# Kernel optimization log

Hardware: AMD Instinct MI355X
Metric: run time of the kernel (lower is better)

The kernel has to match this reference:

```python
import jax, jax.numpy as jnp
import numpy as np

B, S, D, VOCAB, K = 32, 128, 300, 20000, 8


def setup_inputs() -> dict:
    key = jax.random.key(0)
    ks = jax.random.split(key, 12)
    return {
        "words": jax.random.normal(ks[0], (B, S, D), jnp.float32),
        "lengths": jax.random.randint(ks[1], (B,), S // 2, S + 1),
        "vocab": jax.random.normal(ks[2], (VOCAB, D), jnp.float32) * 0.1,
        "default_embed": jax.random.uniform(ks[3], (D,), jnp.float32),
        "W": jnp.eye(D, dtype=jnp.float32) + 0.01 * jax.random.normal(ks[4], (D, D), jnp.float32),
        "lstm_Wih": jax.random.normal(ks[5], (4 * D, D), jnp.float32) * 0.05,
        "lstm_Whh": jax.random.normal(ks[6], (4 * D, D), jnp.float32) * 0.05,
        "lstm_bih": jnp.zeros((4 * D,), jnp.float32),
        "lstm_bhh": jnp.zeros((4 * D,), jnp.float32),
        "rnn_Wih": jax.random.normal(ks[7], (D, D), jnp.float32) * 0.05,
        "rnn_Whh": jax.random.normal(ks[8], (D, D), jnp.float32) * 0.05,
        "rnn_bih": jnp.zeros((D,), jnp.float32),
        "rnn_bhh": jnp.zeros((D,), jnp.float32),
    }


def _forward(words, lengths, vocab, default_embed, W,
             lstm_Wih, lstm_Whh, lstm_bih, lstm_bhh,
             rnn_Wih, rnn_Whh, rnn_bih, rnn_bhh):
    b, s, d = words.shape
    # --- NormalizeWordsModel (tagger) ---
    C = jnp.concatenate([vocab.T, default_embed[:, None]], axis=1)  # [D, V+1]
    P = jax.nn.softmax(jnp.einsum("bsd,de,ev->bsv", words, W, C), axis=-1)  # [B,S,V+1]
    V = P[..., -1:] * words + jnp.einsum("bsv,vd->bsd", P[..., :-1], vocab)  # [B,S,D]

    # --- LSTM encoder, final hidden at true length (packed-sequence semantics) ---
    valid = (jnp.arange(s)[None, :] < lengths[:, None])  # [B,S]

    def lstm_step(carry, xs):
        h, c = carry
        x_t, v_t = xs  # [B,D], [B]
        gates = x_t @ lstm_Wih.T + lstm_bih + h @ lstm_Whh.T + lstm_bhh  # [B,4D]
        i, f, g, o = jnp.split(gates, 4, axis=-1)
        c_new = jax.nn.sigmoid(f) * c + jax.nn.sigmoid(i) * jnp.tanh(g)
        h_new = jax.nn.sigmoid(o) * jnp.tanh(c_new)
        m = v_t[:, None]
        h = jnp.where(m, h_new, h)
        c = jnp.where(m, c_new, c)
        return (h, c), None

    h0 = jnp.zeros((b, d), V.dtype)
    (q, _), _ = jax.lax.scan(lstm_step, (h0, h0),
                             (jnp.swapaxes(V, 0, 1), valid.T))  # q: [B,D]

    # --- InstructionsDecoder: RNNCell applied K times to the same input q ---
    def rnn_step(h, _):
        h2 = jnp.tanh(q @ rnn_Wih.T + rnn_bih + h @ rnn_Whh.T + rnn_bhh)
        return h2, h2

    _, H = jax.lax.scan(rnn_step, h0, None, length=K)  # [K,B,D]
    H = jnp.swapaxes(H, 0, 1)  # [B,K,D]

    # --- masked softmax attention readout ---
    scores = jnp.einsum("bkd,bsd->bks", H, V)  # [B,K,S]
    scores = jnp.where(valid[:, None, :], scores, -jnp.inf)
    R = jnp.einsum("bks,bsd->bkd", jax.nn.softmax(scores, axis=-1), V)
    return R


def reference(words, lengths, vocab, default_embed, W,
              lstm_Wih, lstm_Whh, lstm_bih, lstm_bhh,
              rnn_Wih, rnn_Whh, rnn_bih, rnn_bhh):
    return _forward(words, lengths, vocab, default_embed, W,
                    lstm_Wih, lstm_Whh, lstm_bih, lstm_bhh,
                    rnn_Wih, rnn_Whh, rnn_bih, rnn_bhh)
```

## Files before the change

### kernel.cpp

```cpp
#include <hip/hip_runtime.h>


typedef unsigned short u16;
typedef unsigned int   u32;
typedef float  f32x4 __attribute__((ext_vector_type(4)));
typedef u32    u32x4 __attribute__((ext_vector_type(4)));
typedef __bf16 bf16x8 __attribute__((ext_vector_type(8)));
typedef _Float16 f16x2 __attribute__((ext_vector_type(2)));
typedef _Float16 f16x8 __attribute__((ext_vector_type(8)));

#define SCOPE_AGENT __HIP_MEMORY_SCOPE_AGENT

__device__ __forceinline__ float bf2f(u16 u) { return __uint_as_float(((u32)u) << 16); }
__device__ __forceinline__ u16 f2bf(float f) {
  u32 x = __float_as_uint(f);
  u32 r = (x + 0x7fffu + ((x >> 16) & 1u)) >> 16;
  return (u16)r;
}
__device__ __forceinline__ float sigm(float x) { return 1.f / (1.f + __expf(-x)); }
__device__ __forceinline__ u16 f2h(float f) {
  union { _Float16 h; u16 u; } cv; cv.h = (_Float16)f; return cv.u;
}
__device__ __forceinline__ float h2f(u16 u) {
  union { _Float16 h; u16 u; } cv; cv.u = u; return (float)cv.h;
}

template <int CTRL>
__device__ __forceinline__ float dppmv(float v) {
  return __uint_as_float(
      (u32)__builtin_amdgcn_mov_dpp((int)__float_as_uint(v), CTRL, 0xF, 0xF, true));
}

__device__ __forceinline__ void stage_chunk(const u16* __restrict__ pA,
                                            const u16* __restrict__ pB,
                                            int ci, u16* dst, int tid) {
  const u32x4* gA = (const u32x4*)pA + (size_t)ci * 1280;
  const u32x4* gB = (const u32x4*)pB + (size_t)ci * 1216;
  u32x4* sb = (u32x4*)dst;
#pragma unroll
  for (int i = 0; i < 5; i++) {
    int idx = tid + i * 512;
    if (idx < 2496) {
      const u32x4* g = (idx < 1280) ? (gA + idx) : (gB + (idx - 1280));
      __builtin_amdgcn_global_load_lds(
          (const __attribute__((address_space(1))) u32*)(const u32*)g,
          (__attribute__((address_space(3))) u32*)(u32*)(sb + idx), 16, 0, 0);
    }
  }
}

__device__ __forceinline__ void conv_seg(const void* src, u16* dst, int n, int is32,
                                         int t0, int stride) {
  if (is32) {
    const float* s = (const float*)src;
    for (int i = t0; i < n; i += stride) dst[i] = f2bf(s[i]);
  } else {
    const u16* s = (const u16*)src;
    for (int i = t0; i < n; i += stride) dst[i] = s[i];
  }
}

__global__ __launch_bounds__(256) void k_ingest(
    const void* words, const void* vocab, const void* de, const void* W,
    const void* lWih, const void* lWhh, const void* lbih, const void* lbhh,
    const void* rWih, const void* rWhh, const void* rbih, const void* rbhh,
    u16* cw, u16* cv, u16* cde, u16* cW, u16* cWih, u16* cWhh, u16* cbih, u16* cbhh,
    u16* crWih, u16* crWhh, u16* crbih, u16* crbhh, u32* flag, u32* seqz, u32* hbz) {
  __shared__ int s_is32;
  int tid = threadIdx.x;
  int vote = 0;
  if (tid < 64) {
    u32 w = ((const u32*)words)[tid];
    int e = (w >> 7) & 0xFF;
    vote = (e >= 100 && e <= 150) ? 1 : 0;
  }
  unsigned long long m = __ballot(vote);
  if (tid == 0) s_is32 = (__popcll(m) < 32) ? 1 : 0;
  __syncthreads();
  int is32 = s_is32;
  if (blockIdx.x == 0 && tid == 0) *flag = (u32)is32;
  int t0 = blockIdx.x * 256 + tid;
  int stride = gridDim.x * 256;
  if (t0 < 256) seqz[t0] = 0;
  if (t0 < 10240) hbz[t0] = 0;
  conv_seg(words, cw, 1228800, is32, t0, stride);
  conv_seg(vocab, cv, 6000000, is32, t0, stride);
  conv_seg(de, cde, 300, is32, t0, stride);
  conv_seg(W, cW, 90000, is32, t0, stride);
  conv_seg(lWih, cWih, 360000, is32, t0, stride);
  conv_seg(lWhh, cWhh, 360000, is32, t0, stride);
  conv_seg(lbih, cbih, 1200, is32, t0, stride);
  conv_seg(lbhh, cbhh, 1200, is32, t0, stride);
  conv_seg(rWih, crWih, 90000, is32, t0, stride);
  conv_seg(rWhh, crWhh, 90000, is32, t0, stride);
  conv_seg(rbih, crbih, 300, is32, t0, stride);
  conv_seg(rbhh, crbhh, 300, is32, t0, stride);
}

__global__ __launch_bounds__(256) void k_transpose_bf(const u16* __restrict__ in,
                                                      u16* __restrict__ out,
                                                      int J, int K) {
  __shared__ u16 t[32][33];
  int j0 = blockIdx.x * 32, k0 = blockIdx.y * 32;
  int lx = threadIdx.x & 31, ly = threadIdx.x >> 5;
  for (int r = ly; r < 32; r += 8) {
    int j = j0 + r, k = k0 + lx;
    t[r][lx] = (j < J && k < K) ? in[(size_t)j * K + k] : (u16)0;
  }
  __syncthreads();
  for (int r = ly; r < 32; r += 8) {
    int k = k0 + r, j = j0 + lx;
    if (k < K && j < J) out[(size_t)k * J + j] = t[lx][r];
  }
}

__global__ __launch_bounds__(256) void k_pack_w4(const u16* __restrict__ Whh,
                                                 u16* __restrict__ pW) {
  int idx = blockIdx.x * 256 + threadIdx.x;
  if (idx >= 16 * 25600) return;
  int bid = idx / 25600, r = idx % 25600;
  int t2 = r >> 9, lane = (r >> 3) & 63, j = r & 7;
  int nt = t2 / 10, kt = t2 % 10;
  int n = nt * 16 + (lane & 15);
  int gate = n / 20, dl = n % 20;
  int d0 = (bid < 15) ? 19 * bid : 285;
  int nd = (bid < 15) ? 19 : 15;
  int k = kt * 32 + ((lane >> 4) * 8) + j;
  u16 out = 0;
  if (dl < nd && k < 300) out = f2h(bf2f(Whh[(size_t)(gate * 300 + d0 + dl) * 300 + k]));
  pW[idx] = out;
}

__global__ __launch_bounds__(256) void k_pack_vocab(const u16* __restrict__ vocab,
                                                    u16* __restrict__ pA,
                                                    u16* __restrict__ pB) {
  __shared__ u16 sv[32][320];
  int ci = blockIdx.x, tid = threadIdx.x;
  for (int idx = tid; idx < 32 * 20; idx += 256) {
    int v = idx / 20, k = 300 + (idx - v * 20);
    sv[v][k] = 0;
  }
  for (int idx = tid; idx < 32 * 300; idx += 256) {
    int v = idx / 300, k = idx - v * 300;
    sv[v][k] = vocab[(size_t)(ci * 32 + v) * 300 + k];
  }
  __syncthreads();
  for (int idx = tid; idx < 10240; idx += 256) {
    int j = idx & 7, lane = (idx >> 3) & 63, t2 = idx >> 9;
    int kk = t2 % 10, h = t2 / 10;
    int v = h * 16 + (lane & 15);
    int k = kk * 32 + ((lane >> 4)) * 8 + j;
    pA[(size_t)ci * 10240 + (size_t)idx] = sv[v][k];
  }
  for (int idx = tid; idx < 9728; idx += 256) {
    int j = idx & 7, lane = (idx >> 3) & 63, nc = idx >> 9;
    int v = (lane >> 4) * 8 + j;
    int n = nc * 16 + (lane & 15);
    pB[(size_t)ci * 9728 + (size_t)idx] = sv[v][n];
  }
}

__global__ __launch_bounds__(256) void k_xw(const u16* __restrict__ words,
                                            const u16* __restrict__ W,
                                            u16* __restrict__ X) {
  __shared__ float As[300][33];
  int n0 = blockIdx.x * 128;
  int r0 = blockIdx.y * 32;
  int tid = threadIdx.x;
  for (int idx = tid; idx < 32 * 300; idx += 256) {
    int r = idx / 300, k = idx - r * 300;
    As[k][r] = bf2f(words[(size_t)(r0 + r) * 300 + k]);
  }
  __syncthreads();
  int j = n0 + (tid & 127);
  int rh = (tid >> 7) * 16;
  float acc[16];
#pragma unroll
  for (int i = 0; i < 16; i++) acc[i] = 0.f;
  if (j < 300) {
    for (int k = 0; k < 300; k++) {
      float bw = bf2f(W[(size_t)k * 300 + j]);
#pragma unroll
      for (int i = 0; i < 16; i++) acc[i] += As[k][rh + i] * bw;
    }
  }
  if (j < 320) {
#pragma unroll
    for (int i = 0; i < 16; i++) {
      float v = (j < 300) ? acc[i] : 0.f;
      X[(size_t)(r0 + rh + i) * 320 + j] = f2bf(v);
    }
  }
}

__global__ __launch_bounds__(512, 2) void k_softmax_v(
    const u16* __restrict__ X, const u16* __restrict__ pA, const u16* __restrict__ pB,
    u16* __restrict__ pAcc, float* __restrict__ pML) {
  __shared__ __align__(16) u16 chunk[2][19968];
  __shared__ __align__(16) float ptbuf[8 * 576];
  int bid = blockIdx.x;
  int sl = bid & 7, b = bid >> 3;
  int tid = threadIdx.x;
  int w = tid >> 6, lane = tid & 63;
  int quad = lane >> 4, n16 = lane & 15;
  int cs = (sl == 0) ? 0 : 79 + (sl - 1) * 78;
  int nch = (sl == 0) ? 79 : 78;

  int rowA = b * 128 + w * 16 + n16;
  const bf16x8* Xrow = (const bf16x8*)(X + (size_t)rowA * 320);
  bf16x8 afr[10];
#pragma unroll
  for (int kk = 0; kk < 10; kk++) afr[kk] = Xrow[kk * 4 + quad];

  f32x4 acc[19];
#pragma unroll
  for (int i = 0; i < 19; i++) { acc[i][0] = 0.f; acc[i][1] = 0.f; acc[i][2] = 0.f; acc[i][3] = 0.f; }
  f32x4 mrun, lrun;
#pragma unroll
  for (int c = 0; c < 4; c++) { mrun[c] = -1e30f; lrun[c] = 0.f; }
  float* myPt = ptbuf + w * 576;

  stage_chunk(pA, pB, cs, &chunk[0][0], tid);
  __syncthreads();

  int cur = 0;
  for (int ic = 0; ic < nch; ic++) {
    if (ic + 1 < nch) stage_chunk(pA, pB, cs + ic + 1, &chunk[cur ^ 1][0], tid);
    const bf16x8* bufA = (const bf16x8*)&chunk[cur][0];
    const bf16x8* bufB = (const bf16x8*)&chunk[cur][10240];
    f32x4 L0, L1;
#pragma unroll
    for (int c = 0; c < 4; c++) { L0[c] = 0.f; L1[c] = 0.f; }
#pragma unroll
    for (int kk = 0; kk < 10; kk++) {
      L0 = __builtin_amdgcn_mfma_f32_16x16x32_bf16(afr[kk], bufA[kk * 64 + lane], L0, 0, 0, 0);
      L1 = __builtin_amdgcn_mfma_f32_16x16x32_bf16(afr[kk], bufA[(10 + kk) * 64 + lane], L1, 0, 0, 0);
    }
    f32x4 t;
#pragma unroll
    for (int c = 0; c < 4; c++) {
      float x = fmaxf(L0[c], L1[c]);
      x = fmaxf(x, dppmv<0xB1>(x));
      x = fmaxf(x, dppmv<0x4E>(x));
      x = fmaxf(x, dppmv<0x141>(x));
      x = fmaxf(x, dppmv<0x140>(x));
      t[c] = x;
    }
    f32x4 mnew, al, P0v, P1v, rs;
#pragma unroll
    for (int c = 0; c < 4; c++) {
      mnew[c] = fmaxf(mrun[c], t[c]);
      al[c] = __expf(mrun[c] - mnew[c]);
      P0v[c] = __expf(L0[c] - mnew[c]);
      P1v[c] = __expf(L1[c] - mnew[c]);
      rs[c] = P0v[c] + P1v[c];
    }
#pragma unroll
    for (int c = 0; c < 4; c++) {
      float x = rs[c];
      x += dppmv<0xB1>(x);
      x += dppmv<0x4E>(x);
      x += dppmv<0x141>(x);
      x += dppmv<0x140>(x);
      rs[c] = x;
    }
#pragma unroll
    for (int c = 0; c < 4; c++) { lrun[c] = lrun[c] * al[c] + rs[c]; mrun[c] = mnew[c]; }
#pragma unroll
    for (int r = 0; r < 4; r++) {
      myPt[(quad * 4 + r) * 36 + n16] = P0v[r];
      myPt[(quad * 4 + r) * 36 + 16 + n16] = P1v[r];
    }
    f32x4 plo = *(const f32x4*)(myPt + n16 * 36 + quad * 8);
    f32x4 phi = *(const f32x4*)(myPt + n16 * 36 + quad * 8 + 4);
    bf16x8 paf;
#pragma unroll
    for (int c = 0; c < 4; c++) { paf[c] = (__bf16)plo[c]; paf[c + 4] = (__bf16)phi[c]; }
#pragma unroll
    for (int nc = 0; nc < 19; nc++) {
      f32x4 a = acc[nc];
#pragma unroll
      for (int c = 0; c < 4; c++) a[c] *= al[c];
      acc[nc] = __builtin_amdgcn_mfma_f32_16x16x32_bf16(paf, bufB[nc * 64 + lane], a, 0, 0, 0);
    }
    __syncthreads();
    cur ^= 1;
  }

  size_t prow = (size_t)sl * 4096 + (size_t)b * 128 + w * 16;
  if (n16 == 0) {
#pragma unroll
    for (int r = 0; r < 4; r++) {
      pML[(prow + quad * 4 + r) * 2 + 0] = mrun[r];
      pML[(prow + quad * 4 + r) * 2 + 1] = lrun[r];
    }
  }
#pragma unroll
  for (int nc = 0; nc < 19; nc++)
#pragma unroll
    for (int r = 0; r < 4; r++)
      pAcc[(prow + quad * 4 + r) * 304 + nc * 16 + n16] = f2bf(acc[nc][r]);
}

__global__ __launch_bounds__(320) void k_combine(
    const u16* __restrict__ pAcc, const float* __restrict__ pML,
    const u16* __restrict__ X, const u16* __restrict__ de,
    const u16* __restrict__ words, u16* __restrict__ Vout) {
  __shared__ float red[320];
  __shared__ float fs[8];
  __shared__ float sinv, sw;
  int row = blockIdx.x, tid = threadIdx.x;
  float p = 0.f;
  if (tid < 300) p = bf2f(X[(size_t)row * 320 + tid]) * bf2f(de[tid]);
  red[tid] = p;
  __syncthreads();
  if (tid == 0) {
    float d = 0.f;
    for (int i = 0; i < 300; i++) d += red[i];
    float mv[8], lv[8], ms = -1e30f;
    for (int s = 0; s < 8; s++) {
      mv[s] = pML[((size_t)s * 4096 + row) * 2];
      lv[s] = pML[((size_t)s * 4096 + row) * 2 + 1];
      ms = fmaxf(ms, mv[s]);
    }
    float mf = fmaxf(ms, d);
    float pd = __expf(d - mf);
    float l = pd;
    for (int s = 0; s < 8; s++) {
      float f = __expf(mv[s] - mf);
      fs[s] = f;
      l += lv[s] * f;
    }
    sinv = 1.f / l;
    sw = pd / l;
  }
  __syncthreads();
  float v = 0.f;
  if (tid < 300) {
    float a = 0.f;
#pragma unroll
    for (int s = 0; s < 8; s++)
      a += bf2f(pAcc[((size_t)s * 4096 + row) * 304 + tid]) * fs[s];
    v = a * sinv + sw * bf2f(words[(size_t)row * 300 + tid]);
  }
  Vout[(size_t)row * 320 + tid] = f2bf(v);
}

__global__ __launch_bounds__(256) void k_xg(const u16* __restrict__ Vb,
                                            const u16* __restrict__ WihT,
                                            const u16* __restrict__ bih,
                                            const u16* __restrict__ bhh,
                                            float* __restrict__ xg) {
  __shared__ float As[300][33];
  int n0 = blockIdx.x * 128;
  int r0 = blockIdx.y * 32;
  int tid = threadIdx.x;
  for (int idx = tid; idx < 32 * 300; idx += 256) {
    int r = idx / 300, k = idx - r * 300;
    As[k][r] = bf2f(Vb[(size_t)(r0 + r) * 320 + k]);
  }
  __syncthreads();
  int j = n0 + (tid & 127);
  if (j >= 1200) return;
  int rh = (tid >> 7) * 16;
  float acc[16];
#pragma unroll
  for (int i = 0; i < 16; i++) acc[i] = 0.f;
  for (int k = 0; k < 300; k++) {
    float bw = bf2f(WihT[(size_t)k * 1200 + j]);
#pragma unroll
    for (int i = 0; i < 16; i++) acc[i] += As[k][rh + i] * bw;
  }
  float bias = bf2f(bih[j]) + bf2f(bhh[j]);
#pragma unroll
  for (int i = 0; i < 16; i++)
    xg[(size_t)(r0 + rh + i) * 1200 + j] = acc[i] + bias;
}

__global__ __launch_bounds__(320, 1) void k_lstm2(
    const float* __restrict__ xg, const u16* __restrict__ pW,
    const int* __restrict__ lengths, u16* __restrict__ hb, u32* __restrict__ seq) {
  __shared__ float gl[32][84];
  __shared__ int s_maxlen;
  int bid = blockIdx.x, tid = threadIdx.x;
  int w = tid >> 6, lane = tid & 63;
  int quad = lane >> 4, n16 = lane & 15;
  int d0 = (bid < 15) ? 19 * bid : 285;
  int nd = (bid < 15) ? 19 : 15;
  {
    int lv = (tid < 32) ? lengths[tid] : 0;
    for (int off2 = 1; off2 < 32; off2 <<= 1) {
      int o = __shfl_xor(lv, off2, 64);
      lv = lv > o ? lv : o;
    }
    if (tid == 0) s_maxlen = lv;
  }
  f16x8 bf[10];
  const u32x4* pw4 = (const u32x4*)(pW + (size_t)bid * 25600);
#pragma unroll
  for (int kt = 0; kt < 10; kt++)
    bf[kt] = __builtin_bit_cast(f16x8, pw4[(w * 10 + kt) * 64 + lane]);
  int b0 = tid / 20, dl0 = tid - b0 * 20;
  int b1 = (tid + 320) / 20, dl1 = (tid + 320) - b1 * 20;
  bool a0 = dl0 < nd, a1 = dl1 < nd;
  int len0 = lengths[b0], len1 = lengths[b1];
  int dim0 = d0 + dl0, dim1 = d0 + dl1;
  int sa0 = (((b0 >> 4) * 10 + (dim0 >> 5)) * 64 + ((dim0 >> 3) & 3) * 16 + (b0 & 15)) * 8 + (dim0 & 7);
  int sa1 = (((b1 >> 4) * 10 + (dim1 >> 5)) * 64 + ((dim1 >> 3) & 3) * 16 + (b1 & 15)) * 8 + (dim1 & 7);
  float c0 = 0.f, h0 = 0.f, c1 = 0.f, h1 = 0.f;
  __syncthreads();
  int maxlen = s_maxlen;
  for (int t = 0; t < maxlen; t++) {
    if (tid < 16) {
      while (__hip_atomic_load(&seq[tid * 16], __ATOMIC_ACQUIRE, SCOPE_AGENT) < (u32)t)
        __builtin_amdgcn_s_sleep(2);
    }
    __syncthreads();
    float xv00 = 0.f, xv01 = 0.f, xv02 = 0.f, xv03 = 0.f;
    float xv10 = 0.f, xv11 = 0.f, xv12 = 0.f, xv13 = 0.f;
    const float* xr0 = xg + ((size_t)b0 * 128 + t) * 1200 + dim0;
    const float* xr1 = xg + ((size_t)b1 * 128 + t) * 1200 + dim1;
    if (a0) { xv00 = xr0[0]; xv01 = xr0[300]; xv02 = xr0[600]; xv03 = xr0[900]; }
    if (a1) { xv10 = xr1[0]; xv11 = xr1[300]; xv12 = xr1[600]; xv13 = xr1[900]; }
    const u32x4* hbt = (const u32x4*)hb + (size_t)(t & 1) * 1280;
    u32x4 af[2][10];
#pragma unroll
    for (int mt = 0; mt < 2; mt++)
#pragma unroll
      for (int kt = 0; kt < 10; kt++)
        af[mt][kt] = hbt[(mt * 10 + kt) * 64 + lane];
#pragma unroll
    for (int mt = 0; mt < 2; mt++) {
      f32x4 C;
      C[0] = 0.f; C[1] = 0.f; C[2] = 0.f; C[3] = 0.f;
#pragma unroll
      for (int kt = 0; kt < 10; kt++)
        C = __builtin_amdgcn_mfma_f32_16x16x32_f16(
            __builtin_bit_cast(f16x8, af[mt][kt]), bf[kt], C, 0, 0, 0);
#pragma unroll
      for (int rr = 0; rr < 4; rr++)
        gl[mt * 16 + quad * 4 + rr][w * 16 + n16] = C[rr];
    }
    __syncthreads();
    u16* hbw = hb + (size_t)((t + 1) & 1) * 10240;
    if (a0) {
      float gi = gl[b0][dl0] + xv00, gf = gl[b0][20 + dl0] + xv01;
      float gg = gl[b0][40 + dl0] + xv02, go = gl[b0][60 + dl0] + xv03;
      if (t < len0) {
        c0 = sigm(gf) * c0 + sigm(gi) * tanhf(gg);
        h0 = sigm(go) * tanhf(c0);
      }
      hbw[sa0] = f2h(h0);
    }
    if (a1) {
      float gi = gl[b1][dl1] + xv10, gf = gl[b1][20 + dl1] + xv11;
      float gg = gl[b1][40 + dl1] + xv12, go = gl[b1][60 + dl1] + xv13;
      if (t < len1) {
        c1 = sigm(gf) * c1 + sigm(gi) * tanhf(gg);
        h1 = sigm(go) * tanhf(c1);
      }
      hbw[sa1] = f2h(h1);
    }
    __syncthreads();
    if (tid == 0)
      __hip_atomic_store(&seq[bid * 16], (u32)(t + 1), __ATOMIC_RELEASE, SCOPE_AGENT);
  }
}

__global__ __launch_bounds__(320) void k_rnn(
    const u16* __restrict__ hb, const int* __restrict__ lengths,
    const u16* __restrict__ rWihT, const u16* __restrict__ rWhhT,
    const u16* __restrict__ rbih, const u16* __restrict__ rbhh,
    float* __restrict__ H) {
  __shared__ float qs[304], h2[304], base[304];
  __shared__ int s_maxlen;
  int b = blockIdx.x, tid = threadIdx.x;
  {
    int lv = (tid < 32) ? lengths[tid] : 0;
    for (int off2 = 1; off2 < 32; off2 <<= 1) {
      int o = __shfl_xor(lv, off2, 64);
      lv = lv > o ? lv : o;
    }
    if (tid == 0) s_maxlen = lv;
  }
  __syncthreads();
  int buf = s_maxlen & 1;
  if (tid < 304) {
    float q = 0.f;
    if (tid < 300) {
      int dim = tid;
      int idx = (((b >> 4) * 10 + (dim >> 5)) * 64 + ((dim >> 3) & 3) * 16 + (b & 15)) * 8 + (dim & 7);
      q = h2f(hb[(size_t)buf * 10240 + idx]);
    }
    qs[tid] = q;
    h2[tid] = 0.f;
  }
  __syncthreads();
  if (tid < 300) {
    float a = bf2f(rbih[tid]) + bf2f(rbhh[tid]);
    for (int k = 0; k < 300; k++) a += qs[k] * bf2f(rWihT[(size_t)k * 300 + tid]);
    base[tid] = a;
  }
  __syncthreads();
  for (int s = 0; s < 8; s++) {
    float nv = 0.f;
    if (tid < 300) {
      float a = base[tid];
      for (int k = 0; k < 300; k++) a += h2[k] * bf2f(rWhhT[(size_t)k * 300 + tid]);
      nv = tanhf(a);
    }
    __syncthreads();
    if (tid < 300) {
      h2[tid] = nv;
      H[((size_t)b * 8 + s) * 300 + tid] = nv;
    }
    __syncthreads();
  }
}

__global__ __launch_bounds__(256) void k_attn(const float* __restrict__ H,
                                              const u16* __restrict__ Vb,
                                              const int* __restrict__ lengths,
                                              const u32* __restrict__ flag,
                                              void* __restrict__ dout) {
  __shared__ float Hs[8][304];
  __shared__ float sc[8][128];
  __shared__ float wsum[8];
  int b = blockIdx.x, tid = threadIdx.x;
  int len = lengths[b];
  int is32 = (int)*flag;
  for (int idx = tid; idx < 8 * 300; idx += 256) {
    int k = idx / 300, j = idx - k * 300;
    Hs[k][j] = H[((size_t)b * 8 + k) * 300 + j];
  }
  __syncthreads();
  for (int s = tid; s < len; s += 256) {
    const u16* vr = Vb + (size_t)(b * 128 + s) * 320;
    float a[8];
#pragma unroll
    for (int k = 0; k < 8; k++) a[k] = 0.f;
    for (int j = 0; j < 300; j++) {
      float v = bf2f(vr[j]);
#pragma unroll
      for (int k = 0; k < 8; k++) a[k] += Hs[k][j] * v;
    }
#pragma unroll
    for (int k = 0; k < 8; k++) sc[k][s] = a[k];
  }
  __syncthreads();
  if (tid < 8) {
    float m = -1e30f;
    for (int s = 0; s < len; s++) m = fmaxf(m, sc[tid][s]);
    float l = 0.f;
    for (int s = 0; s < len; s++) { float e = __expf(sc[tid][s] - m); sc[tid][s] = e; l += e; }
    wsum[tid] = 1.f / l;
  }
  __syncthreads();
  int k = tid >> 5, jl = tid & 31;
  for (int j = jl; j < 300; j += 32) {
    float a = 0.f;
    for (int s = 0; s < len; s++) a += sc[k][s] * bf2f(Vb[(size_t)(b * 128 + s) * 320 + j]);
    float val = a * wsum[k];
    size_t o = ((size_t)b * 8 + k) * 300 + j;
    if (is32) ((float*)dout)[o] = val;
    else ((u16*)dout)[o] = f2bf(val);
  }
}

extern "C" void kernel_launch(void* const* d_in, const int* in_sizes, int n_in,
                              void* d_out, int out_size, void* d_ws, size_t ws_size,
                              hipStream_t stream) {
  (void)in_sizes; (void)n_in; (void)out_size; (void)ws_size;
  const void* words = d_in[0];
  const int* lengths = (const int*)d_in[1];
  const void* vocab = d_in[2];
  const void* de = d_in[3];
  const void* W = d_in[4];
  const void* lWih = d_in[5];
  const void* lWhh = d_in[6];
  const void* lbih = d_in[7];
  const void* lbhh = d_in[8];
  const void* rWih = d_in[9];
  const void* rWhh = d_in[10];
  const void* rbih = d_in[11];
  const void* rbhh = d_in[12];

  char* basep = (char*)d_ws;
  size_t off = 0;
  auto take = [&](size_t bytes) -> char* {
    char* p = basep + off;
    off += (bytes + 255) & ~(size_t)255;
    return p;
  };
  u16* cw    = (u16*)take(1228800 * 2);
  u16* cv    = (u16*)take(6000000 * 2);
  u16* cde   = (u16*)take(300 * 2);
  u16* cW    = (u16*)take(90000 * 2);
  u16* cWih  = (u16*)take(360000 * 2);
  u16* cWhh  = (u16*)take(360000 * 2);
  u16* cbih  = (u16*)take(1200 * 2);
  u16* cbhh  = (u16*)take(1200 * 2);
  u16* crWih = (u16*)take(90000 * 2);
  u16* crWhh = (u16*)take(90000 * 2);
  u16* crbih = (u16*)take(300 * 2);
  u16* crbhh = (u16*)take(300 * 2);
  u32* flag  = (u32*)take(256);
  u16*   X     = (u16*)take((size_t)4096 * 320 * 2);
  u16*   Vb    = (u16*)take((size_t)4096 * 320 * 2);
  u16*   WihT  = (u16*)take((size_t)300 * 1200 * 2);
  u16*   pW4   = (u16*)take((size_t)16 * 25600 * 2);
  u16*   rWihT = (u16*)take((size_t)300 * 300 * 2);
  u16*   rWhhT = (u16*)take((size_t)300 * 300 * 2);
  u16*   pAcc  = (u16*)take((size_t)8 * 4096 * 304 * 2);
  float* pML   = (float*)take((size_t)8 * 4096 * 2 * 4);
  float* H     = (float*)take((size_t)32 * 8 * 300 * 4);
  u16*   hb    = (u16*)take((size_t)2 * 10240 * 2);
  u32*   seq   = (u32*)take((size_t)4096 * 4);
  char* ureg = take((size_t)25000192);
  u16*   pA = (u16*)ureg;
  u16*   pB = (u16*)(ureg + (size_t)625 * 10240 * 2);
  float* xg = (float*)ureg;

  k_ingest<<<4096, 256, 0, stream>>>(words, vocab, de, W, lWih, lWhh, lbih, lbhh,
                                     rWih, rWhh, rbih, rbhh,
                                     cw, cv, cde, cW, cWih, cWhh, cbih, cbhh,
                                     crWih, crWhh, crbih, crbhh, flag, seq, (u32*)hb);
  k_transpose_bf<<<dim3(38, 10), 256, 0, stream>>>(cWih, WihT, 1200, 300);
  k_transpose_bf<<<dim3(10, 10), 256, 0, stream>>>(crWih, rWihT, 300, 300);
  k_transpose_bf<<<dim3(10, 10), 256, 0, stream>>>(crWhh, rWhhT, 300, 300);
  k_pack_w4<<<1600, 256, 0, stream>>>(cWhh, pW4);
  k_pack_vocab<<<625, 256, 0, stream>>>(cv, pA, pB);
  k_xw<<<dim3(3, 128), 256, 0, stream>>>(cw, cW, X);
  k_softmax_v<<<256, 512, 0, stream>>>(X, pA, pB, pAcc, pML);
  k_combine<<<4096, 320, 0, stream>>>(pAcc, pML, X, cde, cw, Vb);
  k_xg<<<dim3(10, 128), 256, 0, stream>>>(Vb, WihT, cbih, cbhh, xg);
  k_lstm2<<<16, 320, 0, stream>>>(xg, pW4, lengths, hb, seq);
  k_rnn<<<32, 320, 0, stream>>>(hb, lengths, rWihT, rWhhT, crbih, crbhh, H);
  k_attn<<<32, 256, 0, stream>>>(H, Vb, lengths, flag, d_out);
}
```

Baseline: 1.065 ms.

## Split LSTM recurrence into two independent batch groups of eight blocks

The recurrent LSTM kernel is restructured so the 32 sequences form two independent groups of 16. Each group gets 8 blocks of 640 threads, each block owning 38 hidden dims. Blocks now synchronize only with the 8 blocks of their own group, and each group stops at its own max length. The hidden-state exchange buffer is split per group, and the Whh packing and the RNN kernel's reads are adjusted to match. This cuts the per-step cross-block barrier fan-in and lets the shorter group finish early, in exchange for more threads per block and MFMA tiles padded out to 40 columns per gate.

New measurement: 990.6 us. 1.08x faster.

```diff
diff --git a/kernel.cpp b/kernel.cpp
--- a/kernel.cpp
+++ b/kernel.cpp
@@ -114,20 +114,25 @@
   }
 }
 
-__global__ __launch_bounds__(256) void k_pack_w4(const u16* __restrict__ Whh,
+__global__ __launch_bounds__(256) void k_pack_w8(const u16* __restrict__ Whh,
                                                  u16* __restrict__ pW) {
   int idx = blockIdx.x * 256 + threadIdx.x;
-  if (idx >= 16 * 25600) return;
-  int bid = idx / 25600, r = idx % 25600;
-  int t2 = r >> 9, lane = (r >> 3) & 63, j = r & 7;
-  int nt = t2 / 10, kt = t2 % 10;
-  int n = nt * 16 + (lane & 15);
-  int gate = n / 20, dl = n % 20;
-  int d0 = (bid < 15) ? 19 * bid : 285;
-  int nd = (bid < 15) ? 19 : 15;
-  int k = kt * 32 + ((lane >> 4) * 8) + j;
+  if (idx >= 409600) return;
+  int bid = idx / 51200;
+  int r = idx - bid * 51200;
+  int j = r & 7;
+  int lane = (r >> 3) & 63;
+  int t2 = r >> 9;
+  int kt = t2 % 10, w = t2 / 10;
+  int n16 = lane & 15, quad = lane >> 4;
+  int n = w * 16 + n16;
+  int gate = n / 40, dl = n - gate * 40;
+  int nd = (bid < 7) ? 38 : 34;
+  int dim = 38 * bid + dl;
+  int k = kt * 32 + quad * 8 + j;
   u16 out = 0;
-  if (dl < nd && k < 300) out = f2h(bf2f(Whh[(size_t)(gate * 300 + d0 + dl) * 300 + k]));
+  if (dl < nd && k < 300)
+    out = f2h(bf2f(Whh[(size_t)(gate * 300 + dim) * 300 + k]));
   pW[idx] = out;
 }
 
@@ -377,93 +382,77 @@
     xg[(size_t)(r0 + rh + i) * 1200 + j] = acc[i] + bias;
 }
 
-__global__ __launch_bounds__(320, 1) void k_lstm2(
+__global__ __launch_bounds__(640, 1) void k_lstm7(
     const float* __restrict__ xg, const u16* __restrict__ pW,
     const int* __restrict__ lengths, u16* __restrict__ hb, u32* __restrict__ seq) {
-  __shared__ float gl[32][84];
+  __shared__ float gl[16][164];
   __shared__ int s_maxlen;
-  int bid = blockIdx.x, tid = threadIdx.x;
+  int bidx = blockIdx.x;
+  int mg = bidx >> 3, bid = bidx & 7;
+  int tid = threadIdx.x;
   int w = tid >> 6, lane = tid & 63;
   int quad = lane >> 4, n16 = lane & 15;
-  int d0 = (bid < 15) ? 19 * bid : 285;
-  int nd = (bid < 15) ? 19 : 15;
+  int nd = (bid < 7) ? 38 : 34;
   {
-    int lv = (tid < 32) ? lengths[tid] : 0;
-    for (int off2 = 1; off2 < 32; off2 <<= 1) {
+    int lv = (tid < 16) ? lengths[mg * 16 + tid] : 0;
+    for (int off2 = 1; off2 < 16; off2 <<= 1) {
       int o = __shfl_xor(lv, off2, 64);
       lv = lv > o ? lv : o;
     }
     if (tid == 0) s_maxlen = lv;
   }
   f16x8 bf[10];
-  const u32x4* pw4 = (const u32x4*)(pW + (size_t)bid * 25600);
+  const u32x4* pw4 = (const u32x4*)(pW + (size_t)bid * 51200);
 #pragma unroll
   for (int kt = 0; kt < 10; kt++)
     bf[kt] = __builtin_bit_cast(f16x8, pw4[(w * 10 + kt) * 64 + lane]);
-  int b0 = tid / 20, dl0 = tid - b0 * 20;
-  int b1 = (tid + 320) / 20, dl1 = (tid + 320) - b1 * 20;
-  bool a0 = dl0 < nd, a1 = dl1 < nd;
-  int len0 = lengths[b0], len1 = lengths[b1];
-  int dim0 = d0 + dl0, dim1 = d0 + dl1;
-  int sa0 = (((b0 >> 4) * 10 + (dim0 >> 5)) * 64 + ((dim0 >> 3) & 3) * 16 + (b0 & 15)) * 8 + (dim0 & 7);
-  int sa1 = (((b1 >> 4) * 10 + (dim1 >> 5)) * 64 + ((dim1 >> 3) & 3) * 16 + (b1 & 15)) * 8 + (dim1 & 7);
-  float c0 = 0.f, h0 = 0.f, c1 = 0.f, h1 = 0.f;
+  int b0 = tid / 40, dl = tid - b0 * 40;
+  bool a0 = dl < nd;
+  int bg = mg * 16 + b0;
+  int len0 = lengths[bg];
+  int dim = 38 * bid + dl;
+  int sa = (((dim >> 5)) * 64 + ((dim >> 3) & 3) * 16 + b0) * 8 + (dim & 7);
+  float c0 = 0.f, h0 = 0.f;
+  u32* myf = seq + (size_t)bidx * 16;
   __syncthreads();
   int maxlen = s_maxlen;
   for (int t = 0; t < maxlen; t++) {
-    if (tid < 16) {
-      while (__hip_atomic_load(&seq[tid * 16], __ATOMIC_ACQUIRE, SCOPE_AGENT) < (u32)t)
+    if (tid < 8) {
+      while (__hip_atomic_load(&seq[(mg * 8 + tid) * 16], __ATOMIC_ACQUIRE, SCOPE_AGENT) < (u32)t)
         __builtin_amdgcn_s_sleep(2);
     }
     __syncthreads();
-    float xv00 = 0.f, xv01 = 0.f, xv02 = 0.f, xv03 = 0.f;
-    float xv10 = 0.f, xv11 = 0.f, xv12 = 0.f, xv13 = 0.f;
-    const float* xr0 = xg + ((size_t)b0 * 128 + t) * 1200 + dim0;
-    const float* xr1 = xg + ((size_t)b1 * 128 + t) * 1200 + dim1;
-    if (a0) { xv00 = xr0[0]; xv01 = xr0[300]; xv02 = xr0[600]; xv03 = xr0[900]; }
-    if (a1) { xv10 = xr1[0]; xv11 = xr1[300]; xv12 = xr1[600]; xv13 = xr1[900]; }
-    const u32x4* hbt = (const u32x4*)hb + (size_t)(t & 1) * 1280;
-    u32x4 af[2][10];
-#pragma unroll
-    for (int mt = 0; mt < 2; mt++)
-#pragma unroll
-      for (int kt = 0; kt < 10; kt++)
-        af[mt][kt] = hbt[(mt * 10 + kt) * 64 + lane];
-#pragma unroll
-    for (int mt = 0; mt < 2; mt++) {
-      f32x4 C;
-      C[0] = 0.f; C[1] = 0.f; C[2] = 0.f; C[3] = 0.f;
-#pragma unroll
-      for (int kt = 0; kt < 10; kt++)
-        C = __builtin_amdgcn_mfma_f32_16x16x32_f16(
-            __builtin_bit_cast(f16x8, af[mt][kt]), bf[kt], C, 0, 0, 0);
-#pragma unroll
-      for (int rr = 0; rr < 4; rr++)
-        gl[mt * 16 + quad * 4 + rr][w * 16 + n16] = C[rr];
-    }
+    float xv0 = 0.f, xv1 = 0.f, xv2 = 0.f, xv3 = 0.f;
+    const float* xr0 = xg + ((size_t)bg * 128 + t) * 1200 + dim;
+    if (a0) { xv0 = xr0[0]; xv1 = xr0[300]; xv2 = xr0[600]; xv3 = xr0[900]; }
+    const u32x4* hbt = (const u32x4*)hb + (size_t)(mg * 2 + (t & 1)) * 640;
+    u32x4 af[10];
+#pragma unroll
+    for (int kt = 0; kt < 10; kt++)
+      af[kt] = hbt[kt * 64 + lane];
+    f32x4 C;
+    C[0] = 0.f; C[1] = 0.f; C[2] = 0.f; C[3] = 0.f;
+#pragma unroll
+    for (int kt = 0; kt < 10; kt++)
+      C = __builtin_amdgcn_mfma_f32_16x16x32_f16(
+          __builtin_bit_cast(f16x8, af[kt]), bf[kt], C, 0, 0, 0);
+#pragma unroll
+    for (int rr = 0; rr < 4; rr++)
+      gl[quad * 4 + rr][w * 16 + n16] = C[rr];
     __syncthreads();
-    u16* hbw = hb + (size_t)((t + 1) & 1) * 10240;
+    u16* hbw = hb + (size_t)(mg * 2 + ((t + 1) & 1)) * 5120;
     if (a0) {
-      float gi = gl[b0][dl0] + xv00, gf = gl[b0][20 + dl0] + xv01;
-      float gg = gl[b0][40 + dl0] + xv02, go = gl[b0][60 + dl0] + xv03;
+      float gi = gl[b0][dl] + xv0, gf = gl[b0][40 + dl] + xv1;
+      float gg = gl[b0][80 + dl] + xv2, go = gl[b0][120 + dl] + xv3;
       if (t < len0) {
         c0 = sigm(gf) * c0 + sigm(gi) * tanhf(gg);
         h0 = sigm(go) * tanhf(c0);
       }
-      hbw[sa0] = f2h(h0);
-    }
-    if (a1) {
-      float gi = gl[b1][dl1] + xv10, gf = gl[b1][20 + dl1] + xv11;
-      float gg = gl[b1][40 + dl1] + xv12, go = gl[b1][60 + dl1] + xv13;
-      if (t < len1) {
-        c1 = sigm(gf) * c1 + sigm(gi) * tanhf(gg);
-        h1 = sigm(go) * tanhf(c1);
-      }
-      hbw[sa1] = f2h(h1);
+      hbw[sa] = f2h(h0);
     }
     __syncthreads();
     if (tid == 0)
-      __hip_atomic_store(&seq[bid * 16], (u32)(t + 1), __ATOMIC_RELEASE, SCOPE_AGENT);
+      __hip_atomic_store(myf, (u32)(t + 1), __ATOMIC_RELEASE, SCOPE_AGENT);
   }
 }
 
@@ -475,9 +464,10 @@
   __shared__ float qs[304], h2[304], base[304];
   __shared__ int s_maxlen;
   int b = blockIdx.x, tid = threadIdx.x;
+  int mg = b >> 4;
   {
-    int lv = (tid < 32) ? lengths[tid] : 0;
-    for (int off2 = 1; off2 < 32; off2 <<= 1) {
+    int lv = (tid < 16) ? lengths[mg * 16 + tid] : 0;
+    for (int off2 = 1; off2 < 16; off2 <<= 1) {
       int o = __shfl_xor(lv, off2, 64);
       lv = lv > o ? lv : o;
     }
@@ -489,8 +479,8 @@
     float q = 0.f;
     if (tid < 300) {
       int dim = tid;
-      int idx = (((b >> 4) * 10 + (dim >> 5)) * 64 + ((dim >> 3) & 3) * 16 + (b & 15)) * 8 + (dim & 7);
-      q = h2f(hb[(size_t)buf * 10240 + idx]);
+      int idx = ((dim >> 5) * 64 + ((dim >> 3) & 3) * 16 + (b & 15)) * 8 + (dim & 7);
+      q = h2f(hb[(size_t)(mg * 2 + buf) * 5120 + idx]);
     }
     qs[tid] = q;
     h2[tid] = 0.f;
@@ -608,13 +598,13 @@
   u16*   X     = (u16*)take((size_t)4096 * 320 * 2);
   u16*   Vb    = (u16*)take((size_t)4096 * 320 * 2);
   u16*   WihT  = (u16*)take((size_t)300 * 1200 * 2);
-  u16*   pW4   = (u16*)take((size_t)16 * 25600 * 2);
+  u16*   pW8   = (u16*)take((size_t)409600 * 2);
   u16*   rWihT = (u16*)take((size_t)300 * 300 * 2);
   u16*   rWhhT = (u16*)take((size_t)300 * 300 * 2);
   u16*   pAcc  = (u16*)take((size_t)8 * 4096 * 304 * 2);
   float* pML   = (float*)take((size_t)8 * 4096 * 2 * 4);
   float* H     = (float*)take((size_t)32 * 8 * 300 * 4);
-  u16*   hb    = (u16*)take((size_t)2 * 10240 * 2);
+  u16*   hb    = (u16*)take((size_t)2 * 2 * 5120 * 2);
   u32*   seq   = (u32*)take((size_t)4096 * 4);
   char* ureg = take((size_t)25000192);
   u16*   pA = (u16*)ureg;
@@ -628,13 +618,13 @@
   k_transpose_bf<<<dim3(38, 10), 256, 0, stream>>>(cWih, WihT, 1200, 300);
   k_transpose_bf<<<dim3(10, 10), 256, 0, stream>>>(crWih, rWihT, 300, 300);
   k_transpose_bf<<<dim3(10, 10), 256, 0, stream>>>(crWhh, rWhhT, 300, 300);
-  k_pack_w4<<<1600, 256, 0, stream>>>(cWhh, pW4);
+  k_pack_w8<<<1600, 256, 0, stream>>>(cWhh, pW8);
   k_pack_vocab<<<625, 256, 0, stream>>>(cv, pA, pB);
   k_xw<<<dim3(3, 128), 256, 0, stream>>>(cw, cW, X);
   k_softmax_v<<<256, 512, 0, stream>>>(X, pA, pB, pAcc, pML);
   k_combine<<<4096, 320, 0, stream>>>(pAcc, pML, X, cde, cw, Vb);
   k_xg<<<dim3(10, 128), 256, 0, stream>>>(Vb, WihT, cbih, cbhh, xg);
-  k_lstm2<<<16, 320, 0, stream>>>(xg, pW4, lengths, hb, seq);
+  k_lstm7<<<16, 640, 0, stream>>>(xg, pW8, lengths, hb, seq);
   k_rnn<<<32, 320, 0, stream>>>(hb, lengths, rWihT, rWhhT, crbih, crbhh, H);
   k_attn<<<32, 256, 0, stream>>>(H, Vb, lengths, flag, d_out);
 }
```
